# Optimization experiments

Measured on AMD Instinct MI355X. Metric: run time of the kernel, lower is better.

The kernel has to match this reference:

```python
import jax, jax.numpy as jnp
import numpy as np

E, N_NODES, D, OUT, FDIM = 1_000_000, 50_000, 16, 64, 256


def setup_inputs() -> dict:
    key = jax.random.key(0)
    ks = jax.random.split(key, 16)
    s = 0.1  # param scale (stand-in for xavier init)
    return {
        "Sij": jax.random.uniform(ks[0], (E,), jnp.float32),
        "Cijj": jax.random.normal(ks[1], (E, D, D), jnp.float32),
        "dst": jax.random.randint(ks[2], (E,), 0, N_NODES, dtype=jnp.int32),
        "N": N_NODES,
        "Wc": jax.random.normal(ks[3], (OUT, D), jnp.float32) * s,
        "alphaC": jax.random.normal(ks[4], (D, 1), jnp.float32) * s,
        "alphaf": jax.random.normal(ks[5], (FDIM, 1), jnp.float32) * s,
        "b": jax.random.normal(ks[6], (OUT, 1), jnp.float32) * s,
        "w": jax.random.normal(ks[7], (1, OUT), jnp.float32) * s,
        "Wf": jax.random.normal(ks[8], (OUT, FDIM), jnp.float32) * s,
        "bias": jax.random.normal(ks[9], (OUT, 1), jnp.float32) * s,
        "W1": jax.random.normal(ks[10], (FDIM, D), jnp.float32) * s,
        "b1": jax.random.normal(ks[11], (FDIM,), jnp.float32) * s,
        "W2": jax.random.normal(ks[12], (1, D), jnp.float32) * s,
        "b2": jax.random.normal(ks[13], (1,), jnp.float32) * s,
    }


def reference(Sij, Cijj, dst, N, Wc, alphaC, alphaf, b, w, Wf, bias, W1, b1, W2, b2):
    # apply_edges: per-edge scalar * correlation matrix  -> [E, D, D]
    tmp = Sij[:, None, None] * Cijj
    # update_all: mailbox sum over incoming edges -> per-node correlation [N, D, D]
    corr = jax.ops.segment_sum(tmp, dst, num_segments=N)
    # attention logit per node: w @ (Wc @ corr_i @ alphaC + Wf @ alphaf + b)
    v = corr @ alphaC                                  # [N, D, 1]
    wc_v = jnp.einsum('od,ndk->nok', Wc, v)            # [N, OUT, 1]
    c0 = Wf @ alphaf + b                               # [OUT, 1] (node-independent)
    logits = jnp.einsum('po,nok->n', w, wc_v + c0)     # [N]
    att = jax.nn.softmax(logits)                       # softmax over all nodes
    # Ci = sum_n att_n * corr_n  -> [D, D]
    Ci = jnp.einsum('n,nij->ij', att, corr)
    # small MLP tail
    Fi = jax.nn.sigmoid(jax.nn.relu(Ci @ W1.T + b1))   # [D, FDIM]
    Fi2 = jax.nn.relu(Fi.T @ W2.T + b2)                # [FDIM, 1]
    P = (Wf @ Fi2 + bias).T                            # [1, OUT]
    return P
```

## Files before the change

kernel.cpp:

```cpp
#include <hip/hip_runtime.h>
#include <hip/hip_bf16.h>


#define NNODES 50000

typedef float f32x4 __attribute__((ext_vector_type(4)));

__global__ void k_init(const float* __restrict__ Wc,
                       const float* __restrict__ alphaC,
                       const float* __restrict__ w,
                       float* __restrict__ M,
                       float* __restrict__ logits,
                       float* __restrict__ Ci,
                       int N) {
    int t = blockIdx.x * blockDim.x + threadIdx.x;
    int stride = gridDim.x * blockDim.x;
    for (int i = t; i < N; i += stride) logits[i] = 0.f;
    if (blockIdx.x == 0) {
        __shared__ float wWc[16];
        int tt = threadIdx.x;
        if (tt < 16) {
            float s = 0.f;
            for (int o = 0; o < 64; ++o) s = fmaf(w[o], Wc[o * 16 + tt], s);
            wWc[tt] = s;
        }
        __syncthreads();
        M[tt]  = wWc[tt >> 4] * alphaC[tt & 15];
        Ci[tt] = 0.f;
    }
}

__global__ void k_logits(const float* __restrict__ Sij,
                         const f32x4* __restrict__ C,
                         const int* __restrict__ dst,
                         const float* __restrict__ M,
                         float* __restrict__ logits,
                         int E) {
    int t = blockIdx.x * blockDim.x + threadIdx.x;
    int lane = t & 63;
    int sub  = lane >> 4;
    int eoff = lane & 15;
    int gwid  = t >> 6;
    int waves = (gridDim.x * blockDim.x) >> 6;

    const f32x4* M4 = reinterpret_cast<const f32x4*>(M);
    f32x4 m0 = M4[eoff], m1 = M4[16 + eoff], m2 = M4[32 + eoff], m3 = M4[48 + eoff];

    int nq = (E + 3) >> 2;
    for (int q = gwid; q < nq; q += waves) {
        int e = (q << 2) + sub;
        float d = 0.f;
        if (e < E) {
            size_t base = (size_t)e * 64 + eoff;
            f32x4 c0 = __builtin_nontemporal_load(C + base);
            f32x4 c1 = __builtin_nontemporal_load(C + base + 16);
            f32x4 c2 = __builtin_nontemporal_load(C + base + 32);
            f32x4 c3 = __builtin_nontemporal_load(C + base + 48);
            d = c0[0]*m0[0] + c0[1]*m0[1] + c0[2]*m0[2] + c0[3]*m0[3];
            d = fmaf(c1[0], m1[0], fmaf(c1[1], m1[1], fmaf(c1[2], m1[2], fmaf(c1[3], m1[3], d))));
            d = fmaf(c2[0], m2[0], fmaf(c2[1], m2[1], fmaf(c2[2], m2[2], fmaf(c2[3], m2[3], d))));
            d = fmaf(c3[0], m3[0], fmaf(c3[1], m3[1], fmaf(c3[2], m3[2], fmaf(c3[3], m3[3], d))));
        }
        #pragma unroll
        for (int off = 8; off; off >>= 1) d += __shfl_down(d, off, 16);
        if (eoff == 0 && e < E) atomicAdd(&logits[dst[e]], Sij[e] * d);
    }
}

__global__ void k_softmax(const float* __restrict__ logits,
                          float* __restrict__ att, int N) {
    __shared__ float red[16];
    __shared__ float bval;
    int t = threadIdx.x;
    int nt = blockDim.x;
    int nw = nt >> 6;

    float mx = -1e30f;
    for (int i = t; i < N; i += nt) mx = fmaxf(mx, logits[i]);
    #pragma unroll
    for (int off = 32; off; off >>= 1) mx = fmaxf(mx, __shfl_down(mx, off, 64));
    if ((t & 63) == 0) red[t >> 6] = mx;
    __syncthreads();
    if (t == 0) {
        float m = red[0];
        for (int i = 1; i < nw; ++i) m = fmaxf(m, red[i]);
        bval = m;
    }
    __syncthreads();
    float m = bval;

    float s = 0.f;
    for (int i = t; i < N; i += nt) {
        float e = __expf(logits[i] - m);
        att[i] = e;
        s += e;
    }
    #pragma unroll
    for (int off = 32; off; off >>= 1) s += __shfl_down(s, off, 64);
    __syncthreads();
    if ((t & 63) == 0) red[t >> 6] = s;
    __syncthreads();
    if (t == 0) {
        float ss = 0.f;
        for (int i = 0; i < nw; ++i) ss += red[i];
        bval = ss;
    }
    __syncthreads();
    float inv = 1.f / bval;
    for (int i = t; i < N; i += nt) att[i] *= inv;
}

__global__ void k_ci(const float* __restrict__ Sij,
                     const f32x4* __restrict__ C,
                     const int* __restrict__ dst,
                     const float* __restrict__ att,
                     float* __restrict__ Ci,
                     int E) {
    int t = threadIdx.x;
    int lane = t & 63;
    int sub  = lane >> 4;
    int eoff = lane & 15;
    int gwid  = (blockIdx.x * blockDim.x + t) >> 6;
    int waves = (gridDim.x * blockDim.x) >> 6;

    f32x4 a0 = 0.f, a1 = 0.f, a2 = 0.f, a3 = 0.f;
    int nq = (E + 3) >> 2;
    for (int q = gwid; q < nq; q += waves) {
        int e = (q << 2) + sub;
        if (e < E) {
            float wgt = att[dst[e]] * Sij[e];
            size_t base = (size_t)e * 64 + eoff;
            f32x4 c0 = __builtin_nontemporal_load(C + base);
            f32x4 c1 = __builtin_nontemporal_load(C + base + 16);
            f32x4 c2 = __builtin_nontemporal_load(C + base + 32);
            f32x4 c3 = __builtin_nontemporal_load(C + base + 48);
            a0 += wgt * c0;
            a1 += wgt * c1;
            a2 += wgt * c2;
            a3 += wgt * c3;
        }
    }
    __shared__ f32x4 part[256][4];
    part[t][0] = a0;
    part[t][1] = a1;
    part[t][2] = a2;
    part[t][3] = a3;
    __syncthreads();
    int k  = t & 3;
    int f4 = t >> 2;
    int eo = f4 & 15;
    int j  = f4 >> 4;
    float s = 0.f;
    #pragma unroll
    for (int wv = 0; wv < 4; ++wv)
        #pragma unroll
        for (int sb = 0; sb < 4; ++sb)
            s += part[wv * 64 + sb * 16 + eo][j][k];
    atomicAdd(&Ci[t], s);
}

__global__ void k_tail(const float* __restrict__ Ci,
                       const float* __restrict__ W1,
                       const float* __restrict__ b1,
                       const float* __restrict__ W2,
                       const float* __restrict__ b2,
                       const float* __restrict__ Wf,
                       const float* __restrict__ bias,
                       float* __restrict__ out) {
    __shared__ float ci[256];
    __shared__ float fi2[256];
    int t = threadIdx.x;
    ci[t] = Ci[t];
    __syncthreads();

    float w1row[16];
    #pragma unroll
    for (int j = 0; j < 16; ++j) w1row[j] = W1[t * 16 + j];
    float bb = b1[t];
    float g = 0.f;
    #pragma unroll
    for (int i = 0; i < 16; ++i) {
        float s = bb;
        #pragma unroll
        for (int j = 0; j < 16; ++j) s = fmaf(ci[i * 16 + j], w1row[j], s);
        s = fmaxf(s, 0.f);
        float sg = 1.f / (1.f + __expf(-s));
        g = fmaf(sg, W2[i], g);
    }
    fi2[t] = fmaxf(g + b2[0], 0.f);
    __syncthreads();

    if (t < 64) {
        float s = bias[t];
        for (int f = 0; f < 256; ++f) s = fmaf(Wf[t * 256 + f], fi2[f], s);
        out[t] = s;
    }
}

extern "C" void kernel_launch(void* const* d_in, const int* in_sizes, int n_in,
                              void* d_out, int out_size, void* d_ws, size_t ws_size,
                              hipStream_t stream) {
    const float* Sij    = (const float*)d_in[0];
    const float* Cijj   = (const float*)d_in[1];
    const int*   dst    = (const int*)d_in[2];
    const float* Wc     = (const float*)d_in[4];
    const float* alphaC = (const float*)d_in[5];
    const float* w_     = (const float*)d_in[8];
    const float* Wf     = (const float*)d_in[9];
    const float* bias   = (const float*)d_in[10];
    const float* W1     = (const float*)d_in[11];
    const float* b1     = (const float*)d_in[12];
    const float* W2     = (const float*)d_in[13];
    const float* b2     = (const float*)d_in[14];

    const int E = in_sizes[0];
    const int N = NNODES;

    float* logits = (float*)d_ws;
    float* att    = logits + N;
    float* M      = att + N;
    float* Ci     = M + 256;

    k_init<<<64, 256, 0, stream>>>(Wc, alphaC, w_, M, logits, Ci, N);
    k_logits<<<2048, 256, 0, stream>>>(Sij, (const f32x4*)Cijj, dst, M, logits, E);
    k_softmax<<<1, 1024, 0, stream>>>(logits, att, N);
    k_ci<<<1024, 256, 0, stream>>>(Sij, (const f32x4*)Cijj, dst, att, Ci, E);
    k_tail<<<1, 256, 0, stream>>>(Ci, W1, b1, W2, b2, Wf, bias, (float*)d_out);
}
```

Before: 383.8 us.

## Parallelize softmax across blocks, defer normalization, reverse edge order for cache reuse

The single-block softmax becomes two multi-block kernels: a max reduction that uses an order-preserving unsigned encoding with atomicMax, and an exp/sum pass that accumulates the partition function with atomicAdd. Normalization by Z moves into the tail kernel, so the extra pass over att disappears. The logits kernel switches from nontemporal to regular loads, and the Ci kernel walks edges in reverse, so the tail of Cijj still held in the large last-level cache after the logits pass can be reread without going to HBM. The Ci grid is also doubled. Float atomics make the summation order nondeterministic.

```diff
diff --git a/kernel.cpp b/kernel.cpp
--- a/kernel.cpp
+++ b/kernel.cpp
@@ -5,6 +5,15 @@
 #define NNODES 50000
 
 typedef float f32x4 __attribute__((ext_vector_type(4)));
+
+__device__ __forceinline__ unsigned f2o(float f) {
+    unsigned u = __float_as_uint(f);
+    return (u & 0x80000000u) ? ~u : (u | 0x80000000u);
+}
+__device__ __forceinline__ float o2f(unsigned u) {
+    return (u & 0x80000000u) ? __uint_as_float(u ^ 0x80000000u)
+                             : __uint_as_float(~u);
+}
 
 __global__ void k_init(const float* __restrict__ Wc,
                        const float* __restrict__ alphaC,
@@ -12,6 +21,8 @@
                        float* __restrict__ M,
                        float* __restrict__ logits,
                        float* __restrict__ Ci,
+                       float* __restrict__ Z,
+                       unsigned* __restrict__ mEnc,
                        int N) {
     int t = blockIdx.x * blockDim.x + threadIdx.x;
     int stride = gridDim.x * blockDim.x;
@@ -27,6 +38,7 @@
         __syncthreads();
         M[tt]  = wWc[tt >> 4] * alphaC[tt & 15];
         Ci[tt] = 0.f;
+        if (tt == 0) { Z[0] = 0.f; mEnc[0] = 0u; }
     }
 }
 
@@ -52,10 +64,10 @@
         float d = 0.f;
         if (e < E) {
             size_t base = (size_t)e * 64 + eoff;
-            f32x4 c0 = __builtin_nontemporal_load(C + base);
-            f32x4 c1 = __builtin_nontemporal_load(C + base + 16);
-            f32x4 c2 = __builtin_nontemporal_load(C + base + 32);
-            f32x4 c3 = __builtin_nontemporal_load(C + base + 48);
+            f32x4 c0 = C[base];
+            f32x4 c1 = C[base + 16];
+            f32x4 c2 = C[base + 32];
+            f32x4 c3 = C[base + 48];
             d = c0[0]*m0[0] + c0[1]*m0[1] + c0[2]*m0[2] + c0[3]*m0[3];
             d = fmaf(c1[0], m1[0], fmaf(c1[1], m1[1], fmaf(c1[2], m1[2], fmaf(c1[3], m1[3], d))));
             d = fmaf(c2[0], m2[0], fmaf(c2[1], m2[1], fmaf(c2[2], m2[2], fmaf(c2[3], m2[3], d))));
@@ -67,47 +79,49 @@
     }
 }
 
-__global__ void k_softmax(const float* __restrict__ logits,
-                          float* __restrict__ att, int N) {
-    __shared__ float red[16];
-    __shared__ float bval;
-    int t = threadIdx.x;
-    int nt = blockDim.x;
-    int nw = nt >> 6;
-
+__global__ void k_max(const float* __restrict__ logits,
+                      unsigned* __restrict__ mEnc, int N) {
+    __shared__ float red[4];
+    int t = blockIdx.x * blockDim.x + threadIdx.x;
+    int stride = gridDim.x * blockDim.x;
     float mx = -1e30f;
-    for (int i = t; i < N; i += nt) mx = fmaxf(mx, logits[i]);
+    for (int i = t; i < N; i += stride) mx = fmaxf(mx, logits[i]);
     #pragma unroll
     for (int off = 32; off; off >>= 1) mx = fmaxf(mx, __shfl_down(mx, off, 64));
-    if ((t & 63) == 0) red[t >> 6] = mx;
-    __syncthreads();
-    if (t == 0) {
+    int lt = threadIdx.x;
+    if ((lt & 63) == 0) red[lt >> 6] = mx;
+    __syncthreads();
+    if (lt == 0) {
         float m = red[0];
-        for (int i = 1; i < nw; ++i) m = fmaxf(m, red[i]);
-        bval = m;
-    }
-    __syncthreads();
-    float m = bval;
-
+        for (int i = 1; i < (int)(blockDim.x >> 6); ++i) m = fmaxf(m, red[i]);
+        atomicMax(mEnc, f2o(m));
+    }
+}
+
+__global__ void k_exp(const float* __restrict__ logits,
+                      const unsigned* __restrict__ mEnc,
+                      float* __restrict__ att,
+                      float* __restrict__ Z, int N) {
+    __shared__ float red[4];
+    float m = o2f(*mEnc);
+    int t = blockIdx.x * blockDim.x + threadIdx.x;
+    int stride = gridDim.x * blockDim.x;
     float s = 0.f;
-    for (int i = t; i < N; i += nt) {
+    for (int i = t; i < N; i += stride) {
         float e = __expf(logits[i] - m);
         att[i] = e;
         s += e;
     }
     #pragma unroll
     for (int off = 32; off; off >>= 1) s += __shfl_down(s, off, 64);
-    __syncthreads();
-    if ((t & 63) == 0) red[t >> 6] = s;
-    __syncthreads();
-    if (t == 0) {
+    int lt = threadIdx.x;
+    if ((lt & 63) == 0) red[lt >> 6] = s;
+    __syncthreads();
+    if (lt == 0) {
         float ss = 0.f;
-        for (int i = 0; i < nw; ++i) ss += red[i];
-        bval = ss;
-    }
-    __syncthreads();
-    float inv = 1.f / bval;
-    for (int i = t; i < N; i += nt) att[i] *= inv;
+        for (int i = 0; i < (int)(blockDim.x >> 6); ++i) ss += red[i];
+        atomicAdd(Z, ss);
+    }
 }
 
 __global__ void k_ci(const float* __restrict__ Sij,
@@ -126,7 +140,8 @@
     f32x4 a0 = 0.f, a1 = 0.f, a2 = 0.f, a3 = 0.f;
     int nq = (E + 3) >> 2;
     for (int q = gwid; q < nq; q += waves) {
-        int e = (q << 2) + sub;
+        int qq = nq - 1 - q;
+        int e = (qq << 2) + sub;
         if (e < E) {
             float wgt = att[dst[e]] * Sij[e];
             size_t base = (size_t)e * 64 + eoff;
@@ -160,6 +175,7 @@
 }
 
 __global__ void k_tail(const float* __restrict__ Ci,
+                       const float* __restrict__ Z,
                        const float* __restrict__ W1,
                        const float* __restrict__ b1,
                        const float* __restrict__ W2,
@@ -170,7 +186,8 @@
     __shared__ float ci[256];
     __shared__ float fi2[256];
     int t = threadIdx.x;
-    ci[t] = Ci[t];
+    float invZ = 1.f / Z[0];
+    ci[t] = Ci[t] * invZ;
     __syncthreads();
 
     float w1row[16];
@@ -220,10 +237,13 @@
     float* att    = logits + N;
     float* M      = att + N;
     float* Ci     = M + 256;
-
-    k_init<<<64, 256, 0, stream>>>(Wc, alphaC, w_, M, logits, Ci, N);
+    float* Z      = Ci + 256;
+    unsigned* mEnc = (unsigned*)(Z + 1);
+
+    k_init<<<64, 256, 0, stream>>>(Wc, alphaC, w_, M, logits, Ci, Z, mEnc, N);
     k_logits<<<2048, 256, 0, stream>>>(Sij, (const f32x4*)Cijj, dst, M, logits, E);
-    k_softmax<<<1, 1024, 0, stream>>>(logits, att, N);
-    k_ci<<<1024, 256, 0, stream>>>(Sij, (const f32x4*)Cijj, dst, att, Ci, E);
-    k_tail<<<1, 256, 0, stream>>>(Ci, W1, b1, W2, b2, Wf, bias, (float*)d_out);
-}
+    k_max<<<50, 256, 0, stream>>>(logits, mEnc, N);
+    k_exp<<<50, 256, 0, stream>>>(logits, mEnc, att, Z, N);
+    k_ci<<<2048, 256, 0, stream>>>(Sij, (const f32x4*)Cijj, dst, att, Ci, E);
+    k_tail<<<1, 256, 0, stream>>>(Ci, Z, W1, b1, W2, b2, Wf, bias, (float*)d_out);
+}
```

New measurement: 372.3 us. -3.0%, faster.
